# Optimization experiments

Measured on AMD Instinct MI355X. Metric: run time of the kernel, lower is better.

The kernel has to match this reference:

```python
import jax, jax.numpy as jnp
import numpy as np

B, L, D = 4, 2048, 1024
H, HD = 16, 64
N = 2048  # total number of sets across the batch
TOPK = 8


def setup_inputs() -> dict:
    key = jax.random.key(0)
    ks = jax.random.split(key, 10)
    s = 0.02
    # ragged segment pointers: roughly equal segments with jitter, min length >= TOPK
    rng = np.random.default_rng(0)
    base = N // B
    jit = rng.integers(-base // 4, base // 4, size=B)
    lens = np.maximum(base + jit, TOPK + 1)
    lens = (lens * (N / lens.sum())).astype(np.int64)
    lens[-1] = N - lens[:-1].sum()
    q_ptrs = jnp.asarray(np.concatenate([[0], np.cumsum(lens)]), dtype=jnp.int64)
    return {
        "token_states": jax.random.normal(ks[0], (B, L, D), jnp.float32),
        "Z_sets": jax.random.normal(ks[1], (N, H, HD), jnp.float32),
        "desc_q": jax.random.normal(ks[2], (N, D), jnp.float32),
        "q_ptrs": q_ptrs,
        "Wg_w": jax.random.normal(ks[3], (D, D), jnp.float32) * s,
        "Wg_b": jnp.zeros((D,), jnp.float32),
        "Wd_w": jax.random.normal(ks[4], (D, D), jnp.float32) * s,
        "Wd_b": jnp.zeros((D,), jnp.float32),
        "out_w": jax.random.normal(ks[5], (D, D), jnp.float32) * s,
        "out_b": jnp.zeros((D,), jnp.float32),
    }


def reference(token_states, Z_sets, desc_q, q_ptrs, Wg_w, Wg_b, Wd_w, Wd_b, out_w, out_b):
    Bs, Ls, Ds = token_states.shape
    Ns = desc_q.shape[0]
    S = Ns  # static pad width (upper bound on max segment length)
    starts = q_ptrs[:-1]                       # [B]
    lengths = q_ptrs[1:] - starts              # [B]
    pos = jnp.arange(S)
    idx = jnp.clip(starts[:, None] + pos[None, :], 0, Ns - 1)   # [B,S]
    valid = pos[None, :] < lengths[:, None]                      # [B,S] bool
    desc_pad = jnp.where(valid[..., None], desc_q[idx], 0.0)     # [B,S,D]
    z_pad = jnp.where(valid[..., None, None], Z_sets[idx], 0.0)  # [B,S,H,HD]

    Tproj = token_states @ Wg_w.T + Wg_b                         # [B,L,D]
    Dproj = desc_pad @ Wd_w.T + Wd_b                             # [B,S,D]
    logits = jnp.einsum('bld,bsd->bls', Tproj, Dproj)            # [B,L,S]
    logits = jnp.where(valid[:, None, :], logits, -jnp.inf)

    if TOPK > 0 and S > TOPK:
        vals, tidx = jax.lax.top_k(logits, TOPK)                 # [B,L,K]
        bidx = jnp.arange(Bs)[:, None, None]
        lidx = jnp.arange(Ls)[None, :, None]
        tmp = jnp.full_like(logits, -jnp.inf)
        tmp = tmp.at[bidx, lidx, tidx].set(vals)
        gates = jax.nn.softmax(tmp, axis=-1)
    else:
        gates = jax.nn.softmax(logits, axis=-1)

    mix = jnp.einsum('bls,bshd->blhd', gates, z_pad)             # [B,L,H,HD]
    return mix.reshape(Bs, Ls, Ds) @ out_w.T + out_b
```

## Files before the change

### kernel.cpp

```cpp
#include <hip/hip_runtime.h>
#include <hip/hip_bf16.h>
#include <math.h>

#define BQ    4
#define LQ    2048
#define D_DIM 1024
#define NQ    2048
#define SMAX  1024
#define TOPK  8

typedef __attribute__((ext_vector_type(8))) short          short8;
typedef __attribute__((ext_vector_type(8))) _Float16       half8;
typedef __attribute__((ext_vector_type(4))) float          f32x4;
typedef __attribute__((ext_vector_type(8))) unsigned short ushort8;
typedef __attribute__((ext_vector_type(4))) unsigned short ushort4v;

typedef __attribute__((address_space(3))) void as3_void;
typedef __attribute__((address_space(1))) void as1_void;

__device__ __forceinline__ void gload_lds16(const void* g, void* l) {
    __builtin_amdgcn_global_load_lds((const as1_void*)g, (as3_void*)l, 16, 0, 0);
}

__device__ __forceinline__ unsigned short f2bf(float f) {
    __hip_bfloat16 h = __float2bfloat16(f);
    return *reinterpret_cast<unsigned short*>(&h);
}
__device__ __forceinline__ float bf2f(unsigned short u) {
    unsigned int w = (unsigned int)u << 16;
    return *reinterpret_cast<float*>(&w);
}
__device__ __forceinline__ unsigned short f2h(float f) {
    _Float16 h = (_Float16)f;
    return *reinterpret_cast<unsigned short*>(&h);
}
__device__ __forceinline__ float h2f(unsigned short u) {
    _Float16 h = *reinterpret_cast<_Float16*>(&u);
    return (float)h;
}

__device__ __forceinline__ int swz(int r) { return (r ^ (r >> 2)) & 3; }

#define WAIT_VM0   asm volatile("s_waitcnt vmcnt(0)" ::: "memory")
#define WAIT_VM4   asm volatile("s_waitcnt vmcnt(4)" ::: "memory")
#define WAIT_VM5   asm volatile("s_waitcnt vmcnt(5)" ::: "memory")
#define WAIT_VM6   asm volatile("s_waitcnt vmcnt(6)" ::: "memory")
#define WAIT_LGKM0 asm volatile("s_waitcnt lgkmcnt(0)" ::: "memory")

__global__ __launch_bounds__(256) void k_cvt_all(
    const float* __restrict__ token_states, const float* __restrict__ desc_q,
    const float* __restrict__ Wd_w, const float* __restrict__ out_w,
    const float* __restrict__ Z_sets, const int* __restrict__ q_raw,
    unsigned short* __restrict__ tokenH, unsigned short* __restrict__ tokenL,
    unsigned short* __restrict__ descH,  unsigned short* __restrict__ descL,
    unsigned short* __restrict__ wdh,    unsigned short* __restrict__ owb,
    unsigned short* __restrict__ Zb,     int* __restrict__ qp)
{
    const int blk = blockIdx.x;
    if (blk == 0 && threadIdx.x == 0) {
        bool is64 = (q_raw[1] == 0);
        for (int i = 0; i <= BQ; ++i)
            qp[i] = is64 ? q_raw[2 * i] : q_raw[i];
    }

    const float* in; unsigned short *hi, *lo = nullptr; int local; bool fp16m = true;
    if (blk < 4096)      { in = token_states; hi = tokenH; lo = tokenL; local = blk; }
    else if (blk < 5120) { in = desc_q; hi = descH; lo = descL; local = blk - 4096; }
    else if (blk < 5632) { in = Wd_w;   hi = wdh;   local = blk - 5120; }
    else if (blk < 6144) { in = out_w;  hi = owb;   local = blk - 5632; fp16m = false; }
    else                 { in = Z_sets; hi = Zb;    local = blk - 6144; fp16m = false; }

    int i = (local * 256 + threadIdx.x) * 8;
    float4 v0 = *reinterpret_cast<const float4*>(in + i);
    float4 v1 = *reinterpret_cast<const float4*>(in + i + 4);
    float x[8] = {v0.x, v0.y, v0.z, v0.w, v1.x, v1.y, v1.z, v1.w};
    ushort8 h8, l8;
#pragma unroll
    for (int k = 0; k < 8; ++k) {
        if (fp16m) {
            unsigned short h = f2h(x[k]);
            h8[k] = h;
            l8[k] = f2h(x[k] - h2f(h));
        } else {
            h8[k] = f2bf(x[k]);
        }
    }
    *reinterpret_cast<ushort8*>(hi + i) = h8;
    if (lo) *reinterpret_cast<ushort8*>(lo + i) = l8;
}

__global__ __launch_bounds__(256) void k_wgt(
    const float* __restrict__ Wg, unsigned short* __restrict__ wgT)
{
    __shared__ float t[64][65];
    const int tid = threadIdx.x;
    const int j0 = (blockIdx.x & 15) * 64;
    const int d0 = (blockIdx.x >> 4) * 64;
#pragma unroll
    for (int i = 0; i < 16; ++i) {
        int r = i * 4 + (tid >> 6);
        int c = tid & 63;
        t[r][c] = Wg[(size_t)(d0 + r) * D_DIM + j0 + c];
    }
    __syncthreads();
#pragma unroll
    for (int i = 0; i < 16; ++i) {
        int jj = i * 4 + (tid >> 6);
        int dd = tid & 63;
        wgT[(size_t)(j0 + jj) * D_DIM + d0 + dd] = f2h(t[dd][jj]);
    }
}

__global__ __launch_bounds__(256) void k_dzw(
    const unsigned short* __restrict__ descH, const unsigned short* __restrict__ descL,
    const unsigned short* __restrict__ wdh,
    const float* __restrict__ Wd_b, unsigned short* __restrict__ Dproj16,
    const unsigned short* __restrict__ Zb, const unsigned short* __restrict__ owb,
    unsigned short* __restrict__ ZWb)
{
    constexpr int K = D_DIM, N = D_DIM;
    __shared__ __align__(16) char lds[2 * 24576];

    const int d = blockIdx.x;
    const int sub = d >> 1;
    const int bcol = (sub & 7) * 128;
    const int brow = (sub >> 3) * 128;

    const int tid = threadIdx.x;
    const int ln  = tid & 63;
    const int wid = tid >> 6;
    const int wm  = wid >> 1, wn = wid & 1;
    const int fr  = ln & 15, fs = ln >> 4;
    const int srow = tid >> 2;
    const int sslt = tid & 3;

    const int kk0 = (sslt ^ swz(srow)) << 3;
    const size_t offA0 = (size_t)(brow + srow) * K + kk0;
    const size_t offW0 = (size_t)(bcol + srow) * K + kk0;

    if ((d & 1) == 0) {
        auto stage = [&](char* base, int k0) {
            gload_lds16(descH + offA0 + k0,          base + wid * 1024);
            gload_lds16(descH + offA0 + 64 * K + k0, base + 4096 + wid * 1024);
            gload_lds16(descL + offA0 + k0,          base + 8192 + wid * 1024);
            gload_lds16(descL + offA0 + 64 * K + k0, base + 12288 + wid * 1024);
            gload_lds16(wdh + offW0 + k0,            base + 16384 + wid * 1024);
            gload_lds16(wdh + offW0 + 64 * K + k0,   base + 20480 + wid * 1024);
        };

        f32x4 acc[4][4] = {};
        stage(lds, 0);
        stage(lds + 24576, 32);

        const int NT = K / 32;
        for (int t = 0; t < NT; ++t) {
            if (t < NT - 1) { WAIT_VM6; } else { WAIT_VM0; }
            __builtin_amdgcn_s_barrier();

            char* base = lds + (t & 1) * 24576;
            half8 ahf[4], alf[4], bhf[4];
#pragma unroll
            for (int mi = 0; mi < 4; ++mi) {
                int r = wm * 64 + mi * 16 + fr;
                int o = r * 64 + ((fs ^ swz(r)) << 4);
                ahf[mi] = *reinterpret_cast<const half8*>(base + o);
                alf[mi] = *reinterpret_cast<const half8*>(base + 8192 + o);
            }
#pragma unroll
            for (int ni = 0; ni < 4; ++ni) {
                int c = wn * 64 + ni * 16 + fr;
                int o = c * 64 + ((fs ^ swz(c)) << 4);
                bhf[ni] = *reinterpret_cast<const half8*>(base + 16384 + o);
            }
            __builtin_amdgcn_s_setprio(1);
#pragma unroll
            for (int mi = 0; mi < 4; ++mi)
#pragma unroll
                for (int ni = 0; ni < 4; ++ni)
                    acc[mi][ni] = __builtin_amdgcn_mfma_f32_16x16x32_f16(
                        ahf[mi], bhf[ni], acc[mi][ni], 0, 0, 0);
#pragma unroll
            for (int mi = 0; mi < 4; ++mi)
#pragma unroll
                for (int ni = 0; ni < 4; ++ni)
                    acc[mi][ni] = __builtin_amdgcn_mfma_f32_16x16x32_f16(
                        alf[mi], bhf[ni], acc[mi][ni], 0, 0, 0);
            __builtin_amdgcn_s_setprio(0);

            WAIT_LGKM0;
            __builtin_amdgcn_s_barrier();
            if (t + 2 < NT) stage(base, (t + 2) * 32);
        }

        float bv[4];
#pragma unroll
        for (int ni = 0; ni < 4; ++ni)
            bv[ni] = Wd_b[bcol + wn * 64 + ni * 16 + fr];

#pragma unroll
        for (int mi = 0; mi < 4; ++mi) {
#pragma unroll
            for (int reg = 0; reg < 4; ++reg) {
                int row = brow + wm * 64 + mi * 16 + fs * 4 + reg;
#pragma unroll
                for (int ni = 0; ni < 4; ++ni) {
                    int col = bcol + wn * 64 + ni * 16 + fr;
                    Dproj16[(size_t)row * N + col] = f2h(acc[mi][ni][reg] + bv[ni]);
                }
            }
        }
    } else {
        auto stage = [&](char* base, int k0) {
            gload_lds16(Zb + offA0 + k0,           base + wid * 1024);
            gload_lds16(Zb + offA0 + 64 * K + k0,  base + 4096 + wid * 1024);
            gload_lds16(owb + offW0 + k0,          base + 8192 + wid * 1024);
            gload_lds16(owb + offW0 + 64 * K + k0, base + 12288 + wid * 1024);
        };

        f32x4 acc[4][4] = {};
        stage(lds, 0);
        stage(lds + 24576, 32);

        const int NT = K / 32;
        for (int t = 0; t < NT; ++t) {
            if (t < NT - 1) { WAIT_VM4; } else { WAIT_VM0; }
            __builtin_amdgcn_s_barrier();

            char* base = lds + (t & 1) * 24576;
            short8 a[4], b[4];
#pragma unroll
            for (int mi = 0; mi < 4; ++mi) {
                int r = wm * 64 + mi * 16 + fr;
                a[mi] = *reinterpret_cast<const short8*>(base + r * 64 + ((fs ^ swz(r)) << 4));
            }
#pragma unroll
            for (int ni = 0; ni < 4; ++ni) {
                int c = wn * 64 + ni * 16 + fr;
                b[ni] = *reinterpret_cast<const short8*>(base + 8192 + c * 64 + ((fs ^ swz(c)) << 4));
            }
            __builtin_amdgcn_s_setprio(1);
#pragma unroll
            for (int mi = 0; mi < 4; ++mi)
#pragma unroll
                for (int ni = 0; ni < 4; ++ni)
                    acc[mi][ni] = __builtin_amdgcn_mfma_f32_16x16x32_bf16(
                        a[mi], b[ni], acc[mi][ni], 0, 0, 0);
            __builtin_amdgcn_s_setprio(0);

            WAIT_LGKM0;
            __builtin_amdgcn_s_barrier();
            if (t + 2 < NT) stage(base, (t + 2) * 32);
        }

#pragma unroll
        for (int mi = 0; mi < 4; ++mi) {
#pragma unroll
            for (int reg = 0; reg < 4; ++reg) {
                int row = brow + wm * 64 + mi * 16 + fs * 4 + reg;
#pragma unroll
                for (int ni = 0; ni < 4; ++ni) {
                    int col = bcol + wn * 64 + ni * 16 + fr;
                    ZWb[(size_t)row * N + col] = f2bf(acc[mi][ni][reg]);
                }
            }
        }
    }
}

__global__ __launch_bounds__(256) void k_g(
    const unsigned short* __restrict__ A, const unsigned short* __restrict__ W,
    unsigned short* __restrict__ C, int M, int N, int K)
{
    __shared__ __align__(16) char lds[2 * 16384];

    const int nbx = gridDim.x;
    const int total = nbx * gridDim.y;
    const int d = blockIdx.x + nbx * blockIdx.y;
    const int logical = (d & 7) * (total >> 3) + (d >> 3);
    const int bcol = (logical % nbx) * 128;
    const int brow = (logical / nbx) * 128;

    const int tid = threadIdx.x;
    const int ln  = tid & 63;
    const int wid = tid >> 6;
    const int wm  = wid >> 1, wn = wid & 1;
    const int fr  = ln & 15, fs = ln >> 4;
    const int srow = tid >> 2;
    const int sslt = tid & 3;

    const int kk0 = (sslt ^ swz(srow)) << 3;
    const size_t offA0 = (size_t)(brow + srow) * K + kk0;
    const size_t offW0 = (size_t)(bcol + srow) * K + kk0;

    auto stage = [&](char* base, int k0) {
        gload_lds16(A + offA0 + k0,          base + wid * 1024);
        gload_lds16(A + offA0 + 64 * K + k0, base + 4096 + wid * 1024);
        gload_lds16(W + offW0 + k0,          base + 8192 + wid * 1024);
        gload_lds16(W + offW0 + 64 * K + k0, base + 12288 + wid * 1024);
    };

    f32x4 acc[4][4] = {};

    stage(lds, 0);
    stage(lds + 16384, 32);

    const int NT = K / 32;
    for (int t = 0; t < NT; ++t) {
        if (t < NT - 1) { WAIT_VM4; } else { WAIT_VM0; }
        __builtin_amdgcn_s_barrier();

        char* base = lds + (t & 1) * 16384;
        half8 a[4], b[4];
#pragma unroll
        for (int mi = 0; mi < 4; ++mi) {
            int r = wm * 64 + mi * 16 + fr;
            a[mi] = *reinterpret_cast<const half8*>(base + r * 64 + ((fs ^ swz(r)) << 4));
        }
#pragma unroll
        for (int ni = 0; ni < 4; ++ni) {
            int c = wn * 64 + ni * 16 + fr;
            b[ni] = *reinterpret_cast<const half8*>(base + 8192 + c * 64 + ((fs ^ swz(c)) << 4));
        }
        __builtin_amdgcn_s_setprio(1);
#pragma unroll
        for (int mi = 0; mi < 4; ++mi)
#pragma unroll
            for (int ni = 0; ni < 4; ++ni)
                acc[mi][ni] = __builtin_amdgcn_mfma_f32_16x16x32_f16(
                    a[mi], b[ni], acc[mi][ni], 0, 0, 0);
        __builtin_amdgcn_s_setprio(0);

        WAIT_LGKM0;
        __builtin_amdgcn_s_barrier();
        if (t + 2 < NT) stage(base, (t + 2) * 32);
    }

#pragma unroll
    for (int mi = 0; mi < 4; ++mi) {
#pragma unroll
        for (int reg = 0; reg < 4; ++reg) {
            int row = brow + wm * 64 + mi * 16 + fs * 4 + reg;
#pragma unroll
            for (int ni = 0; ni < 4; ++ni) {
                int col = bcol + wn * 64 + ni * 16 + fr;
                C[(size_t)row * N + col] = f2h(acc[mi][ni][reg]);
            }
        }
    }
}

__global__ __launch_bounds__(256) void k_cvec(
    const unsigned short* __restrict__ Dproj16, const float* __restrict__ bg,
    float* __restrict__ c)
{
    const int row = blockIdx.x * 4 + (threadIdx.x >> 6);
    const int ln  = threadIdx.x & 63;
    const unsigned short* dr = Dproj16 + (size_t)row * D_DIM + ln * 16;
    float s = 0.f;
#pragma unroll
    for (int h = 0; h < 2; ++h) {
        ushort8 v = *reinterpret_cast<const ushort8*>(dr + h * 8);
#pragma unroll
        for (int j = 0; j < 8; ++j)
            s = fmaf(bg[ln * 16 + h * 8 + j], h2f(v[j]), s);
    }
#pragma unroll
    for (int off = 32; off > 0; off >>= 1)
        s += __shfl_xor(s, off);
    if (ln == 0) c[row] = s;
}

__global__ __launch_bounds__(256) void k_logits_2p(
    const unsigned short* __restrict__ TH, const unsigned short* __restrict__ TL,
    const unsigned short* __restrict__ G16, const float* __restrict__ cvec,
    const int* __restrict__ qp, float* __restrict__ logits)
{
    const int d = blockIdx.x + 16 * (blockIdx.y + 16 * blockIdx.z);
    const int logical = (d & 7) * 128 + (d >> 3);
    const int b    = logical >> 8;
    const int brow = ((logical >> 4) & 15) * 128;
    const int bcol = (logical & 15) * 64;

    const int start = qp[b], len = qp[b + 1] - start;
    if (bcol >= len) return;

    __shared__ __align__(16) char lds[2 * 20480];

    const int tid = threadIdx.x;
    const int ln  = tid & 63;
    const int wid = tid >> 6;
    const int fr  = ln & 15, fs = ln >> 4;
    const int srow = tid >> 2;
    const int sslt = tid & 3;

    const int kka = (sslt ^ swz(srow)) << 3;
    const size_t offA0 = ((size_t)b * LQ + brow + srow) * D_DIM + kka;
    int wr = start + bcol + srow; if (wr > NQ - 1) wr = NQ - 1;
    const size_t offW0 = (size_t)wr * D_DIM + kka;

    auto stage = [&](char* base, int k0) {
        gload_lds16(TH + offA0 + k0,              base + wid * 1024);
        gload_lds16(TH + offA0 + 64 * D_DIM + k0, base + 4096 + wid * 1024);
        gload_lds16(TL + offA0 + k0,              base + 8192 + wid * 1024);
        gload_lds16(TL + offA0 + 64 * D_DIM + k0, base + 12288 + wid * 1024);
        gload_lds16(G16 + offW0 + k0,             base + 16384 + wid * 1024);
    };

    f32x4 acc[2][4] = {};

    stage(lds, 0);
    stage(lds + 20480, 32);

    const int NT = D_DIM / 32;
    for (int t = 0; t < NT; ++t) {
        if (t < NT - 1) { WAIT_VM5; } else { WAIT_VM0; }
        __builtin_amdgcn_s_barrier();

        char* base = lds + (t & 1) * 20480;
        half8 ah[2], al[2], bf[4];
#pragma unroll
        for (int mi = 0; mi < 2; ++mi) {
            int r = wid * 32 + mi * 16 + fr;
            int o = r * 64 + ((fs ^ swz(r)) << 4);
            ah[mi] = *reinterpret_cast<const half8*>(base + o);
            al[mi] = *reinterpret_cast<const half8*>(base + 8192 + o);
        }
#pragma unroll
        for (int ni = 0; ni < 4; ++ni) {
            int c = ni * 16 + fr;
            bf[ni] = *reinterpret_cast<const half8*>(base + 16384 + c * 64 + ((fs ^ swz(c)) << 4));
        }
        __builtin_amdgcn_s_setprio(1);
#pragma unroll
        for (int mi = 0; mi < 2; ++mi)
#pragma unroll
            for (int ni = 0; ni < 4; ++ni)
                acc[mi][ni] = __builtin_amdgcn_mfma_f32_16x16x32_f16(
                    ah[mi], bf[ni], acc[mi][ni], 0, 0, 0);
#pragma unroll
        for (int mi = 0; mi < 2; ++mi)
#pragma unroll
            for (int ni = 0; ni < 4; ++ni)
                acc[mi][ni] = __builtin_amdgcn_mfma_f32_16x16x32_f16(
                    al[mi], bf[ni], acc[mi][ni], 0, 0, 0);
        __builtin_amdgcn_s_setprio(0);

        WAIT_LGKM0;
        __builtin_amdgcn_s_barrier();
        if (t + 2 < NT) stage(base, (t + 2) * 32);
    }

    float cv[4];
#pragma unroll
    for (int ni = 0; ni < 4; ++ni) {
        int ci = start + bcol + ni * 16 + fr;
        if (ci > NQ - 1) ci = NQ - 1;
        cv[ni] = cvec[ci];
    }

#pragma unroll
    for (int mi = 0; mi < 2; ++mi) {
#pragma unroll
        for (int reg = 0; reg < 4; ++reg) {
            size_t row = (size_t)b * LQ + brow + wid * 32 + mi * 16 + fs * 4 + reg;
#pragma unroll
            for (int ni = 0; ni < 4; ++ni) {
                int col = bcol + ni * 16 + fr;
                logits[row * SMAX + col] = acc[mi][ni][reg] + cv[ni];
            }
        }
    }
}

__global__ __launch_bounds__(256) void k_topk_out(
    const float* __restrict__ logits, const unsigned short* __restrict__ ZW,
    const float* __restrict__ out_b, const int* __restrict__ qp,
    float* __restrict__ out)
{
    const int ln  = threadIdx.x & 63;
    const int row = blockIdx.x * 4 + (threadIdx.x >> 6);
    const int b   = row >> 11;
    const int start = qp[b], len = qp[b + 1] - start;

    const float* lrow = logits + (size_t)row * SMAX;

    float v[16];
#pragma unroll
    for (int c = 0; c < 4; ++c) {
        float4 q = reinterpret_cast<const float4*>(lrow)[c * 64 + ln];
        int s0 = c * 256 + ln * 4;
        v[c * 4 + 0] = (s0 + 0 < len) ? q.x : -INFINITY;
        v[c * 4 + 1] = (s0 + 1 < len) ? q.y : -INFINITY;
        v[c * 4 + 2] = (s0 + 2 < len) ? q.z : -INFINITY;
        v[c * 4 + 3] = (s0 + 3 < len) ? q.w : -INFINITY;
    }

    float wv[TOPK]; int wi[TOPK];
#pragma unroll
    for (int it = 0; it < TOPK; ++it) {
        float bvv = v[0]; int bj = 0;
#pragma unroll
        for (int j = 1; j < 16; ++j)
            if (v[j] > bvv) { bvv = v[j]; bj = j; }
        int gidx = (bj >> 2) * 256 + ln * 4 + (bj & 3);
        float cv = bvv; int ci = gidx;
#pragma unroll
        for (int off = 32; off > 0; off >>= 1) {
            float ov = __shfl_xor(cv, off);
            int   oi = __shfl_xor(ci, off);
            if (ov > cv || (ov == cv && oi < ci)) { cv = ov; ci = oi; }
        }
        wv[it] = cv; wi[it] = ci;
#pragma unroll
        for (int j = 0; j < 16; ++j) {
            int sj = (j >> 2) * 256 + ln * 4 + (j & 3);
            if (sj == ci) v[j] = -INFINITY;
        }
    }

    float m = wv[0], denom = 0.f;
    float g[TOPK];
#pragma unroll
    for (int k = 0; k < TOPK; ++k) { g[k] = expf(wv[k] - m); denom += g[k]; }
    float inv = 1.f / denom;

    float4 acc[4];
#pragma unroll
    for (int c = 0; c < 4; ++c)
        acc[c] = reinterpret_cast<const float4*>(out_b)[c * 64 + ln];

#pragma unroll
    for (int k = 0; k < TOPK; ++k) {
        int si = wi[k] >= 0 ? wi[k] : 0;
        const ushort4v* zr = reinterpret_cast<const ushort4v*>(
            ZW + (size_t)(start + si) * D_DIM);
        float wgt = g[k] * inv;
#pragma unroll
        for (int c = 0; c < 4; ++c) {
            ushort4v z = zr[c * 64 + ln];
            acc[c].x = fmaf(wgt, bf2f(z[0]), acc[c].x);
            acc[c].y = fmaf(wgt, bf2f(z[1]), acc[c].y);
            acc[c].z = fmaf(wgt, bf2f(z[2]), acc[c].z);
            acc[c].w = fmaf(wgt, bf2f(z[3]), acc[c].w);
        }
    }
    float* orow = out + (size_t)row * D_DIM;
#pragma unroll
    for (int c = 0; c < 4; ++c)
        reinterpret_cast<float4*>(orow)[c * 64 + ln] = acc[c];
}

extern "C" void kernel_launch(void* const* d_in, const int* in_sizes, int n_in,
                              void* d_out, int out_size, void* d_ws, size_t ws_size,
                              hipStream_t stream) {
    const float* token_states = (const float*)d_in[0];
    const float* Z_sets       = (const float*)d_in[1];
    const float* desc_q       = (const float*)d_in[2];
    const int*   q_raw        = (const int*)d_in[3];
    const float* Wg_w  = (const float*)d_in[4];
    const float* Wg_b  = (const float*)d_in[5];
    const float* Wd_w  = (const float*)d_in[6];
    const float* Wd_b  = (const float*)d_in[7];
    const float* out_w = (const float*)d_in[8];
    const float* out_b = (const float*)d_in[9];
    float* out = (float*)d_out;

    const size_t NTOK = (size_t)BQ * LQ * D_DIM;
    const size_t NDES = (size_t)NQ * D_DIM;
    const size_t NW   = (size_t)D_DIM * D_DIM;

    char* ws = (char*)d_ws;
    int* qp = (int*)ws;
    unsigned short* tokenH  = (unsigned short*)(ws + 256);
    unsigned short* tokenL  = tokenH + NTOK;
    unsigned short* descH   = tokenL + NTOK;
    unsigned short* descL   = descH + NDES;
    unsigned short* wdh     = descL + NDES;
    unsigned short* wgT     = wdh + NW;
    unsigned short* owb     = wgT + NW;
    unsigned short* Zb      = owb + NW;
    unsigned short* Dproj16 = Zb + NDES;
    unsigned short* ZWb     = Dproj16 + NDES;
    unsigned short* G16     = ZWb + NDES;
    float* cvec             = (float*)(G16 + NDES);
    float* logit            = cvec + 2048;

    k_cvt_all<<<7168, 256, 0, stream>>>(
        token_states, desc_q, Wd_w, out_w, Z_sets, q_raw,
        tokenH, tokenL, descH, descL, wdh, owb, Zb, qp);

    k_wgt<<<256, 256, 0, stream>>>(Wg_w, wgT);

    k_dzw<<<256, 256, 0, stream>>>(
        descH, descL, wdh, Wd_b, Dproj16, Zb, owb, ZWb);

    k_g<<<dim3(8, 16), 256, 0, stream>>>(Dproj16, wgT, G16, NQ, D_DIM, D_DIM);

    k_cvec<<<512, 256, 0, stream>>>(Dproj16, Wg_b, cvec);

    k_logits_2p<<<dim3(SMAX / 64, LQ / 128, BQ), 256, 0, stream>>>(
        tokenH, tokenL, G16, cvec, qp, logit);

    k_topk_out<<<(BQ * LQ) / 4, 256, 0, stream>>>(logit, ZWb, out_b, qp, out);
}
```

Measured before the change: 136.7 us.

## Compact logits grid over valid column tiles and halve row tile size

A tile map built in k_cvec lists only the 64-column tiles that fall inside each batch segment, so the logits kernel launches a dense grid over valid tiles instead of launching the full padded grid and returning early. The row tile also shrinks from 128 to 64 rows, which lowers LDS use and register pressure and gives more blocks for occupancy. The trade-off is that G16 tiles are reused across fewer rows, so B-operand traffic per FLOP doubles, and the map is built serially by a single thread.

```diff
diff --git a/kernel.cpp b/kernel.cpp
--- a/kernel.cpp
+++ b/kernel.cpp
@@ -42,8 +42,8 @@
 __device__ __forceinline__ int swz(int r) { return (r ^ (r >> 2)) & 3; }
 
 #define WAIT_VM0   asm volatile("s_waitcnt vmcnt(0)" ::: "memory")
+#define WAIT_VM3   asm volatile("s_waitcnt vmcnt(3)" ::: "memory")
 #define WAIT_VM4   asm volatile("s_waitcnt vmcnt(4)" ::: "memory")
-#define WAIT_VM5   asm volatile("s_waitcnt vmcnt(5)" ::: "memory")
 #define WAIT_VM6   asm volatile("s_waitcnt vmcnt(6)" ::: "memory")
 #define WAIT_LGKM0 asm volatile("s_waitcnt lgkmcnt(0)" ::: "memory")
 
@@ -351,8 +351,19 @@
 
 __global__ __launch_bounds__(256) void k_cvec(
     const unsigned short* __restrict__ Dproj16, const float* __restrict__ bg,
-    float* __restrict__ c)
+    const int* __restrict__ qp, int* __restrict__ tmap, float* __restrict__ c)
 {
+    if (blockIdx.x == 0 && threadIdx.x == 0) {
+        int idx = 0;
+        for (int b = 0; b < BQ; ++b) {
+            int len = qp[b + 1] - qp[b];
+            int nt = (len + 63) >> 6;
+            for (int j = 0; j < nt; ++j)
+                tmap[idx++] = (b << 16) | (j * 64);
+        }
+        tmap[40] = idx;
+    }
+
     const int row = blockIdx.x * 4 + (threadIdx.x >> 6);
     const int ln  = threadIdx.x & 63;
     const unsigned short* dr = Dproj16 + (size_t)row * D_DIM + ln * 16;
@@ -373,18 +384,20 @@
 __global__ __launch_bounds__(256) void k_logits_2p(
     const unsigned short* __restrict__ TH, const unsigned short* __restrict__ TL,
     const unsigned short* __restrict__ G16, const float* __restrict__ cvec,
-    const int* __restrict__ qp, float* __restrict__ logits)
+    const int* __restrict__ qp, const int* __restrict__ tmap,
+    float* __restrict__ logits)
 {
-    const int d = blockIdx.x + 16 * (blockIdx.y + 16 * blockIdx.z);
-    const int logical = (d & 7) * 128 + (d >> 3);
-    const int b    = logical >> 8;
-    const int brow = ((logical >> 4) & 15) * 128;
-    const int bcol = (logical & 15) * 64;
-
-    const int start = qp[b], len = qp[b + 1] - start;
-    if (bcol >= len) return;
-
-    __shared__ __align__(16) char lds[2 * 20480];
+    const int d = blockIdx.x + 40 * blockIdx.y;
+    const int logical = (d & 7) * 160 + (d >> 3);
+    const int t0   = logical % 40;
+    const int brow = (logical / 40) * 64;
+    if (t0 >= tmap[40]) return;
+    const int m    = tmap[t0];
+    const int b    = m >> 16;
+    const int bcol = m & 0xffff;
+    const int start = qp[b];
+
+    __shared__ __align__(16) char lds[2 * 12288];
 
     const int tid = threadIdx.x;
     const int ln  = tid & 63;
@@ -399,50 +412,41 @@
     const size_t offW0 = (size_t)wr * D_DIM + kka;
 
     auto stage = [&](char* base, int k0) {
-        gload_lds16(TH + offA0 + k0,              base + wid * 1024);
-        gload_lds16(TH + offA0 + 64 * D_DIM + k0, base + 4096 + wid * 1024);
-        gload_lds16(TL + offA0 + k0,              base + 8192 + wid * 1024);
-        gload_lds16(TL + offA0 + 64 * D_DIM + k0, base + 12288 + wid * 1024);
-        gload_lds16(G16 + offW0 + k0,             base + 16384 + wid * 1024);
+        gload_lds16(TH + offA0 + k0,  base + wid * 1024);
+        gload_lds16(TL + offA0 + k0,  base + 4096 + wid * 1024);
+        gload_lds16(G16 + offW0 + k0, base + 8192 + wid * 1024);
     };
 
-    f32x4 acc[2][4] = {};
+    f32x4 acc[4] = {};
 
     stage(lds, 0);
-    stage(lds + 20480, 32);
+    stage(lds + 12288, 32);
 
     const int NT = D_DIM / 32;
     for (int t = 0; t < NT; ++t) {
-        if (t < NT - 1) { WAIT_VM5; } else { WAIT_VM0; }
+        if (t < NT - 1) { WAIT_VM3; } else { WAIT_VM0; }
         __builtin_amdgcn_s_barrier();
 
-        char* base = lds + (t & 1) * 20480;
-        half8 ah[2], al[2], bf[4];
-#pragma unroll
-        for (int mi = 0; mi < 2; ++mi) {
-            int r = wid * 32 + mi * 16 + fr;
+        char* base = lds + (t & 1) * 12288;
+        half8 ah, al, bf[4];
+        {
+            int r = wid * 16 + fr;
             int o = r * 64 + ((fs ^ swz(r)) << 4);
-            ah[mi] = *reinterpret_cast<const half8*>(base + o);
-            al[mi] = *reinterpret_cast<const half8*>(base + 8192 + o);
+            ah = *reinterpret_cast<const half8*>(base + o);
+            al = *reinterpret_cast<const half8*>(base + 4096 + o);
         }
 #pragma unroll
         for (int ni = 0; ni < 4; ++ni) {
-            int c = ni * 16 + fr;
-            bf[ni] = *reinterpret_cast<const half8*>(base + 16384 + c * 64 + ((fs ^ swz(c)) << 4));
+            int cc = ni * 16 + fr;
+            bf[ni] = *reinterpret_cast<const half8*>(base + 8192 + cc * 64 + ((fs ^ swz(cc)) << 4));
         }
         __builtin_amdgcn_s_setprio(1);
 #pragma unroll
-        for (int mi = 0; mi < 2; ++mi)
-#pragma unroll
-            for (int ni = 0; ni < 4; ++ni)
-                acc[mi][ni] = __builtin_amdgcn_mfma_f32_16x16x32_f16(
-                    ah[mi], bf[ni], acc[mi][ni], 0, 0, 0);
-#pragma unroll
-        for (int mi = 0; mi < 2; ++mi)
-#pragma unroll
-            for (int ni = 0; ni < 4; ++ni)
-                acc[mi][ni] = __builtin_amdgcn_mfma_f32_16x16x32_f16(
-                    al[mi], bf[ni], acc[mi][ni], 0, 0, 0);
+        for (int ni = 0; ni < 4; ++ni)
+            acc[ni] = __builtin_amdgcn_mfma_f32_16x16x32_f16(ah, bf[ni], acc[ni], 0, 0, 0);
+#pragma unroll
+        for (int ni = 0; ni < 4; ++ni)
+            acc[ni] = __builtin_amdgcn_mfma_f32_16x16x32_f16(al, bf[ni], acc[ni], 0, 0, 0);
         __builtin_amdgcn_s_setprio(0);
 
         WAIT_LGKM0;
@@ -459,15 +463,12 @@
     }
 
 #pragma unroll
-    for (int mi = 0; mi < 2; ++mi) {
-#pragma unroll
-        for (int reg = 0; reg < 4; ++reg) {
-            size_t row = (size_t)b * LQ + brow + wid * 32 + mi * 16 + fs * 4 + reg;
-#pragma unroll
-            for (int ni = 0; ni < 4; ++ni) {
-                int col = bcol + ni * 16 + fr;
-                logits[row * SMAX + col] = acc[mi][ni][reg] + cv[ni];
-            }
+    for (int reg = 0; reg < 4; ++reg) {
+        size_t row = (size_t)b * LQ + brow + wid * 16 + fs * 4 + reg;
+#pragma unroll
+        for (int ni = 0; ni < 4; ++ni) {
+            int col = bcol + ni * 16 + fr;
+            logits[row * SMAX + col] = acc[ni][reg] + cv[ni];
         }
     }
 }
@@ -570,7 +571,8 @@
     const size_t NW   = (size_t)D_DIM * D_DIM;
 
     char* ws = (char*)d_ws;
-    int* qp = (int*)ws;
+    int* qp   = (int*)ws;
+    int* tmap = (int*)(ws + 64);
     unsigned short* tokenH  = (unsigned short*)(ws + 256);
     unsigned short* tokenL  = tokenH + NTOK;
     unsigned short* descH   = tokenL + NTOK;
@@ -596,10 +598,10 @@
 
     k_g<<<dim3(8, 16), 256, 0, stream>>>(Dproj16, wgT, G16, NQ, D_DIM, D_DIM);
 
-    k_cvec<<<512, 256, 0, stream>>>(Dproj16, Wg_b, cvec);
-
-    k_logits_2p<<<dim3(SMAX / 64, LQ / 128, BQ), 256, 0, stream>>>(
-        tokenH, tokenL, G16, cvec, qp, logit);
+    k_cvec<<<512, 256, 0, stream>>>(Dproj16, Wg_b, qp, tmap, cvec);
+
+    k_logits_2p<<<dim3(40, 32), 256, 0, stream>>>(
+        tokenH, tokenL, G16, cvec, qp, tmap, logit);
 
     k_topk_out<<<(BQ * LQ) / 4, 256, 0, stream>>>(logit, ZWb, out_b, qp, out);
 }
```

After: 133.6 us. 1.02x faster.
